# Performance work log

Hardware: AMD Instinct MI355X
Metric: run time of the kernel (lower is better)

Reference implementation:

```python
import jax, jax.numpy as jnp
import numpy as np

N_LOCAL = 16                      # top-k cone hits per (anchor, query)
COS_TH = float(np.cos(np.pi / 12))  # cone half-angle threshold: th = pi / cone_angle_th, cone_angle_th=12


def setup_inputs() -> dict:
    key = jax.random.key(0)
    k1, k2, k3 = jax.random.split(key, 3)
    pcd = jax.random.normal(k1, (2, 2048, 3), dtype=jnp.float32)  # point cloud
    qry = jax.random.normal(k2, (2, 512, 3), dtype=jnp.float32)   # query points
    anc = jax.random.normal(k3, (2, 48, 3), dtype=jnp.float32)    # anchors
    return {"pcd": pcd, "qry": qry, "anc": anc}


def reference(pcd, qry, anc):
    """Cone-cast top-k neighbor search + relative-feature computation of ARONetModel
    (cast_cone + cal_relatives with norm_coord=False), fully vectorized over anchors.

    Returns a single packed array [b, n_qry, n_anc, 1 + n_local, 4]:
      slot 0 along axis 3 is feat_anc2qry, slots 1..k are feat_qry2hit.
    """
    # ---- cast_cone (vectorized over the anchor loop of the original) ----
    # anchor->point distances/directions do NOT depend on the query, so compute once.
    vec_ap = pcd[:, None, :, :] - anc[:, :, None, :]            # [b,a,p,3]
    dist_ap = jnp.linalg.norm(vec_ap, axis=-1)                  # [b,a,p]
    dir_ap = vec_ap / dist_ap[..., None]                        # [b,a,p,3]

    vec_aq = qry[:, None, :, :] - anc[:, :, None, :]            # [b,a,q,3]
    dir_aq = vec_aq / jnp.linalg.norm(vec_aq, axis=-1, keepdims=True)

    # cosine between anchor->query ray and anchor->point directions
    cos = jnp.einsum('baqd,bapd->baqp', dir_aq, dir_ap)         # [b,a,q,p]
    # points outside the cone get distance +inf (torch: mod[flt_angle] = inf)
    masked = jnp.where(cos <= COS_TH, jnp.inf, dist_ap[:, :, None, :])  # [b,a,q,p]

    neg_vals, idx = jax.lax.top_k(-masked, N_LOCAL)             # smallest-k distances
    vals = -neg_vals                                            # [b,a,q,k]

    # gather the hit point coordinates
    hit_raw = jnp.take_along_axis(pcd[:, None, None, :, :], idx[..., None], axis=3)  # [b,a,q,k,3]
    # padded (no valid point in cone) -> replace with the query point itself
    pad = jnp.isinf(vals)[..., None]                            # [b,a,q,k,1]
    hit = jnp.where(pad, qry[:, None, :, None, :], hit_raw)     # [b,a,q,k,3]
    hit = jnp.transpose(hit, (0, 2, 1, 3, 4))                   # [b,q,a,k,3]

    # ---- cal_relatives (norm_coord = False) ----
    vec_qa = qry[:, :, None, :] - anc[:, None, :, :]            # [b,q,a,3]
    mod_qa = jnp.linalg.norm(vec_qa, axis=-1, keepdims=True)    # [b,q,a,1]
    feat_anc2qry = jnp.concatenate([vec_qa, mod_qa], axis=-1)   # [b,q,a,4]

    vec_qh = hit - qry[:, :, None, None, :]                     # [b,q,a,k,3]
    sq = jnp.sum(vec_qh * vec_qh, axis=-1, keepdims=True)       # [b,q,a,k,1]
    zero = sq == 0.0                                            # padded hits -> exact zero
    mod_qh = jnp.where(zero, 0.0, jnp.sqrt(jnp.where(zero, 1.0, sq)))
    feat_qry2hit = jnp.concatenate([vec_qh, mod_qh], axis=-1)   # [b,q,a,k,4]

    # pack both outputs into one array: [b,q,a,1+k,4]
    return jnp.concatenate([feat_anc2qry[:, :, :, None, :], feat_qry2hit], axis=3)
```

## Files before the change

### kernel.cpp

```cpp
#include <hip/hip_runtime.h>

#define P_N 2048
#define Q_N 512
#define A_N 48
#define NW 4
#define WPTS (P_N / NW)
#define CHUNK 256
#define CAP 32

__device__ __forceinline__ float dot3_rn(float ax, float ay, float az,
                                         float bx, float by, float bz) {
    return __fadd_rn(__fadd_rn(__fmul_rn(ax, bx), __fmul_rn(ay, by)),
                     __fmul_rn(az, bz));
}

__device__ __forceinline__ float dot3_fma(float ax, float ay, float az,
                                          float bx, float by, float bz) {
    return __fmaf_rn(az, bz, __fmaf_rn(ay, by, __fmul_rn(ax, bx)));
}

__device__ __forceinline__ void insert16(float d, int idx, float (&td)[16], int (&ti)[16]) {
    if (d >= td[15]) return;
    #pragma unroll
    for (int j = 15; j >= 1; --j) {
        float oldd = td[j]; int oldi = ti[j];
        bool up   = (d < td[j - 1]);
        bool here = (d < oldd);
        td[j] = up ? td[j - 1] : (here ? d : oldd);
        ti[j] = up ? ti[j - 1] : (here ? idx : oldi);
    }
    if (d < td[0]) { ti[0] = idx; td[0] = d; }
}

__global__ __launch_bounds__(256, 3) void aronet_kernel(
        const float* __restrict__ pcd, const float* __restrict__ qry,
        const float* __restrict__ anc, float* __restrict__ out) {
    __shared__ float4 spt[P_N];
    __shared__ float  scratch_f[4896];

    unsigned short* cand = (unsigned short*)scratch_f;
    float*          mdist = scratch_f;
    unsigned short* midx  = (unsigned short*)(scratch_f + 3264);

    const int tid  = threadIdx.x;
    const int lane = tid & 63;
    const int w    = tid >> 6;

    const int bid = blockIdx.x;
    const int qc  = bid & 7;
    const int ba  = bid >> 3;
    const int a   = ba % A_N;
    const int b   = ba / A_N;

    const float ax = anc[(b * A_N + a) * 3 + 0];
    const float ay = anc[(b * A_N + a) * 3 + 1];
    const float az = anc[(b * A_N + a) * 3 + 2];

    const float* pbase = pcd + (size_t)b * P_N * 3;
    const int pq0 = w * WPTS;
    for (int i = lane; i < WPTS; i += 64) {
        const int p = pq0 + i;
        float vx = __fsub_rn(pbase[p * 3 + 0], ax);
        float vy = __fsub_rn(pbase[p * 3 + 1], ay);
        float vz = __fsub_rn(pbase[p * 3 + 2], az);
        float d2 = dot3_rn(vx, vy, vz, vx, vy, vz);
        float dist = __fsqrt_rn(d2);
        float r = __fdiv_rn(1.0f, dist);
        spt[p] = make_float4(dist, __fmul_rn(vx, r), __fmul_rn(vy, r), __fmul_rn(vz, r));
    }

    const int q = (qc << 6) + lane;
    const float qx = qry[((size_t)b * Q_N + q) * 3 + 0];
    const float qy = qry[((size_t)b * Q_N + q) * 3 + 1];
    const float qz = qry[((size_t)b * Q_N + q) * 3 + 2];
    const float vqx = __fsub_rn(qx, ax);
    const float vqy = __fsub_rn(qy, ay);
    const float vqz = __fsub_rn(qz, az);
    const float qd2 = dot3_rn(vqx, vqy, vqz, vqx, vqy, vqz);
    const float qdist = __fsqrt_rn(qd2);
    const float qr = __fdiv_rn(1.0f, qdist);
    const float dqx = __fmul_rn(vqx, qr);
    const float dqy = __fmul_rn(vqy, qr);
    const float dqz = __fmul_rn(vqz, qr);

    const float COS_TH = 0.9659258262890683f;

    float td[16]; int ti[16];
    #pragma unroll
    for (int j = 0; j < 16; ++j) { td[j] = __builtin_inff(); ti[j] = 0; }

    const int lbase = tid * 33;
    int cnt = 0;
    for (int c0 = pq0; c0 < pq0 + WPTS; c0 += CHUNK) {
        #pragma unroll 4
        for (int p = c0; p < c0 + CHUNK; ++p) {
            float4 pt = spt[p];
            float cosv = dot3_fma(dqx, dqy, dqz, pt.y, pt.z, pt.w);
            if (!(cosv <= COS_TH)) {
                if (cnt < CAP) { cand[lbase + cnt] = (unsigned short)p; cnt++; }
                else insert16(pt.x, p, td, ti);
            }
        }
        for (int k = 0; k < cnt; ++k) {
            int i = cand[lbase + k];
            insert16(spt[i].x, i, td, ti);
        }
        cnt = 0;
    }

    __syncthreads();
    if (w > 0) {
        const int mb = ((w - 1) * 64 + lane) * 17;
        #pragma unroll
        for (int k = 0; k < 16; ++k) {
            mdist[mb + k] = td[k];
            midx [mb + k] = (unsigned short)ti[k];
        }
    }
    __syncthreads();

    if (w == 0) {
        for (int w2 = 0; w2 < NW - 1; ++w2) {
            const int mb = (w2 * 64 + lane) * 17;
            #pragma unroll
            for (int k = 0; k < 16; ++k) {
                float d = mdist[mb + k];
                if (d < __builtin_inff()) insert16(d, (int)midx[mb + k], td, ti);
            }
        }

        float4* o = (float4*)(out + (((size_t)(b * Q_N + q) * A_N + a) * 17) * 4);
        o[0] = make_float4(vqx, vqy, vqz, qdist);

        #pragma unroll
        for (int j = 0; j < 16; ++j) {
            float4 wv;
            if (td[j] == __builtin_inff()) {
                wv = make_float4(0.0f, 0.0f, 0.0f, 0.0f);
            } else {
                const float* hp = pbase + (size_t)ti[j] * 3;
                float hx = __fsub_rn(hp[0], qx);
                float hy = __fsub_rn(hp[1], qy);
                float hz = __fsub_rn(hp[2], qz);
                float sq = dot3_rn(hx, hy, hz, hx, hy, hz);
                float md = (sq == 0.0f) ? 0.0f : __fsqrt_rn(sq);
                wv = make_float4(hx, hy, hz, md);
            }
            o[1 + j] = wv;
        }
    }
}

extern "C" void kernel_launch(void* const* d_in, const int* in_sizes, int n_in,
                              void* d_out, int out_size, void* d_ws, size_t ws_size,
                              hipStream_t stream) {
    const float* pcd = (const float*)d_in[0];
    const float* qry = (const float*)d_in[1];
    const float* anc = (const float*)d_in[2];
    float* out = (float*)d_out;

    dim3 grid(2 * A_N * 8);
    dim3 block(256);
    hipLaunchKernelGGL(aronet_kernel, grid, block, 0, stream, pcd, qry, anc, out);
}
```

Baseline: 192.8 us.

## Split point scan across eight waves with tree merge of per-wave top-k

Block size doubles to 512 threads so each query's 2048 points are scanned by eight waves of 256 points instead of four waves of 512. The partial top-16 lists are then combined by a three-level pairwise tree merge through shared memory, which replaces the serial merge in wave 0. The candidate buffer is cut to 17 entries and flushed whenever it fills, instead of falling back to direct insertion. This shortens each thread's serial scan and merge at the cost of more barriers and higher register and LDS pressure per block.

New measurement: 480.7 us. 149% more time.

```diff
diff --git a/kernel.cpp b/kernel.cpp
--- a/kernel.cpp
+++ b/kernel.cpp
@@ -3,10 +3,10 @@
 #define P_N 2048
 #define Q_N 512
 #define A_N 48
-#define NW 4
-#define WPTS (P_N / NW)
-#define CHUNK 256
-#define CAP 32
+#define NW 8
+#define WPTS 256
+#define CAP 17
+#define FCHUNK 128
 
 __device__ __forceinline__ float dot3_rn(float ax, float ay, float az,
                                          float bx, float by, float bz) {
@@ -32,15 +32,13 @@
     if (d < td[0]) { ti[0] = idx; td[0] = d; }
 }
 
-__global__ __launch_bounds__(256, 3) void aronet_kernel(
+__global__ __launch_bounds__(512, 6) void aronet_kernel(
         const float* __restrict__ pcd, const float* __restrict__ qry,
         const float* __restrict__ anc, float* __restrict__ out) {
-    __shared__ float4 spt[P_N];
-    __shared__ float  scratch_f[4896];
-
-    unsigned short* cand = (unsigned short*)scratch_f;
-    float*          mdist = scratch_f;
-    unsigned short* midx  = (unsigned short*)(scratch_f + 3264);
+    __shared__ float4 spt[NW * WPTS];
+    __shared__ unsigned short cand[512 * CAP];
+
+    uint2* mbuf = (uint2*)spt;
 
     const int tid  = threadIdx.x;
     const int lane = tid & 63;
@@ -52,9 +50,9 @@
     const int a   = ba % A_N;
     const int b   = ba / A_N;
 
-    const float ax = anc[(b * A_N + a) * 3 + 0];
-    const float ay = anc[(b * A_N + a) * 3 + 1];
-    const float az = anc[(b * A_N + a) * 3 + 2];
+    const float ax = anc[ba * 3 + 0];
+    const float ay = anc[ba * 3 + 1];
+    const float az = anc[ba * 3 + 2];
 
     const float* pbase = pcd + (size_t)b * P_N * 3;
     const int pq0 = w * WPTS;
@@ -89,44 +87,88 @@
     #pragma unroll
     for (int j = 0; j < 16; ++j) { td[j] = __builtin_inff(); ti[j] = 0; }
 
-    const int lbase = tid * 33;
+    const int lbase = tid * CAP;
     int cnt = 0;
-    for (int c0 = pq0; c0 < pq0 + WPTS; c0 += CHUNK) {
-        #pragma unroll 4
-        for (int p = c0; p < c0 + CHUNK; ++p) {
-            float4 pt = spt[p];
-            float cosv = dot3_fma(dqx, dqy, dqz, pt.y, pt.z, pt.w);
-            if (!(cosv <= COS_TH)) {
-                if (cnt < CAP) { cand[lbase + cnt] = (unsigned short)p; cnt++; }
-                else insert16(pt.x, p, td, ti);
+    for (int c0 = 0; c0 < WPTS; c0 += FCHUNK) {
+        for (int i0 = c0; i0 < c0 + FCHUNK; i0 += 4) {
+            float4 p0 = spt[pq0 + i0 + 0];
+            float4 p1 = spt[pq0 + i0 + 1];
+            float4 p2 = spt[pq0 + i0 + 2];
+            float4 p3 = spt[pq0 + i0 + 3];
+            #pragma unroll
+            for (int u = 0; u < 4; ++u) {
+                float4 pt = (u == 0) ? p0 : (u == 1) ? p1 : (u == 2) ? p2 : p3;
+                float cosv = dot3_fma(dqx, dqy, dqz, pt.y, pt.z, pt.w);
+                if (!(cosv <= COS_TH)) {
+                    if (cnt == CAP) {
+                        for (int k = 0; k < CAP; ++k) {
+                            int i = cand[lbase + k];
+                            insert16(spt[pq0 + i].x, pq0 + i, td, ti);
+                        }
+                        cnt = 0;
+                    }
+                    cand[lbase + cnt] = (unsigned short)(i0 + u);
+                    ++cnt;
+                }
             }
         }
         for (int k = 0; k < cnt; ++k) {
             int i = cand[lbase + k];
-            insert16(spt[i].x, i, td, ti);
+            insert16(spt[pq0 + i].x, pq0 + i, td, ti);
         }
         cnt = 0;
     }
 
     __syncthreads();
-    if (w > 0) {
-        const int mb = ((w - 1) * 64 + lane) * 17;
+    if (w & 1) {
+        uint2* mb = mbuf + (w >> 1) * 1024;
+        #pragma unroll
+        for (int k = 0; k < 16; ++k)
+            mb[k * 64 + lane] = make_uint2(__float_as_uint(td[k]), (unsigned)ti[k]);
+    }
+    __syncthreads();
+    if (!(w & 1)) {
+        const uint2* mb = mbuf + (w >> 1) * 1024;
         #pragma unroll
         for (int k = 0; k < 16; ++k) {
-            mdist[mb + k] = td[k];
-            midx [mb + k] = (unsigned short)ti[k];
-        }
+            uint2 e = mb[k * 64 + lane];
+            float d = __uint_as_float(e.x);
+            if (d < __builtin_inff()) insert16(d, (int)e.y, td, ti);
+        }
+    }
+    __syncthreads();
+    if (w == 2 || w == 6) {
+        uint2* mb = mbuf + (w >> 2) * 1024;
+        #pragma unroll
+        for (int k = 0; k < 16; ++k)
+            mb[k * 64 + lane] = make_uint2(__float_as_uint(td[k]), (unsigned)ti[k]);
+    }
+    __syncthreads();
+    if (w == 0 || w == 4) {
+        const uint2* mb = mbuf + (w >> 2) * 1024;
+        #pragma unroll
+        for (int k = 0; k < 16; ++k) {
+            uint2 e = mb[k * 64 + lane];
+            float d = __uint_as_float(e.x);
+            if (d < __builtin_inff()) insert16(d, (int)e.y, td, ti);
+        }
+    }
+    __syncthreads();
+    if (w == 4) {
+        uint2* mb = mbuf;
+        #pragma unroll
+        for (int k = 0; k < 16; ++k)
+            mb[k * 64 + lane] = make_uint2(__float_as_uint(td[k]), (unsigned)ti[k]);
     }
     __syncthreads();
 
     if (w == 0) {
-        for (int w2 = 0; w2 < NW - 1; ++w2) {
-            const int mb = (w2 * 64 + lane) * 17;
-            #pragma unroll
-            for (int k = 0; k < 16; ++k) {
-                float d = mdist[mb + k];
-                if (d < __builtin_inff()) insert16(d, (int)midx[mb + k], td, ti);
-            }
+        const uint2* mb = mbuf;
+        #pragma unroll
+        for (int k = 0; k < 16; ++k) {
+            uint2 e = mb[k * 64 + lane];
+            float d = __uint_as_float(e.x);
+            if (d < __builtin_inff()) insert16(d, (int)e.y, td, ti);
         }
 
         float4* o = (float4*)(out + (((size_t)(b * Q_N + q) * A_N + a) * 17) * 4);
@@ -160,6 +202,6 @@
     float* out = (float*)d_out;
 
     dim3 grid(2 * A_N * 8);
-    dim3 block(256);
+    dim3 block(512);
     hipLaunchKernelGGL(aronet_kernel, grid, block, 0, stream, pcd, qry, anc, out);
 }
```
